# Performance work log

Hardware: AMD Instinct MI355X
Metric: run time of the kernel (lower is better)

The kernel has to match this reference:

```python
import jax, jax.numpy as jnp
import numpy as np

L, C, CZ, H = 2048, 512, 16, 16
D = C // H
EPS = 1e-5


def _ln(x, g, b):
    mu = jnp.mean(x, axis=-1, keepdims=True)
    var = jnp.var(x, axis=-1, keepdims=True)
    return (x - mu) * jax.lax.rsqrt(var + EPS) * g + b


def _adaln(x, cond, ln_g, ln_b, w, b):
    # cond: [C] -> scale/shift broadcast over L
    ss = cond @ w + b                      # [2C]
    scale, shift = ss[:C], ss[C:]
    return _ln(x, ln_g, ln_b) * (1.0 + scale) + shift


def setup_inputs() -> dict:
    key = jax.random.key(0)
    ks = jax.random.split(key, 16)
    s = 0.02
    return {
        "x": jax.random.normal(ks[0], (L, C), jnp.float32),
        "pair": jax.random.normal(ks[1], (L, L, CZ), jnp.float32),
        "time_cond": jax.random.normal(ks[2], (C,), jnp.float32),
        "ln1_g": jnp.ones((C,), jnp.float32),
        "ln1_b": jnp.zeros((C,), jnp.float32),
        "ada1_w": jax.random.normal(ks[3], (C, 2 * C), jnp.float32) * s,
        "ada1_b": jnp.zeros((2 * C,), jnp.float32),
        "Wq": jax.random.normal(ks[4], (C, C), jnp.float32) * s,
        "Wk": jax.random.normal(ks[5], (C, C), jnp.float32) * s,
        "Wv": jax.random.normal(ks[6], (C, C), jnp.float32) * s,
        "Wpb": jax.random.normal(ks[7], (CZ, H), jnp.float32) * s,
        "Wo": jax.random.normal(ks[8], (C, C), jnp.float32) * s,
        "bo": jnp.zeros((C,), jnp.float32),
        "ln2_g": jnp.ones((C,), jnp.float32),
        "ln2_b": jnp.zeros((C,), jnp.float32),
        "ada2_w": jax.random.normal(ks[9], (C, 2 * C), jnp.float32) * s,
        "ada2_b": jnp.zeros((2 * C,), jnp.float32),
        "W1": jax.random.normal(ks[10], (C, 4 * C), jnp.float32) * s,
        "b1": jnp.zeros((4 * C,), jnp.float32),
        "W2": jax.random.normal(ks[11], (4 * C, C), jnp.float32) * s,
        "b2": jnp.zeros((C,), jnp.float32),
    }


def reference(x, pair, time_cond, ln1_g, ln1_b, ada1_w, ada1_b,
              Wq, Wk, Wv, Wpb, Wo, bo,
              ln2_g, ln2_b, ada2_w, ada2_b, W1, b1, W2, b2):
    h = _adaln(x, time_cond, ln1_g, ln1_b, ada1_w, ada1_b)        # [L, C]
    q = (h @ Wq).reshape(L, H, D)
    k = (h @ Wk).reshape(L, H, D)
    v = (h @ Wv).reshape(L, H, D)
    scores = jnp.einsum('ihd,jhd->hij', q, k) / jnp.sqrt(jnp.float32(D))
    scores = scores + jnp.einsum('ijz,zh->hij', pair, Wpb)         # pair bias
    attn = jax.nn.softmax(scores, axis=-1)                          # [H, L, L]
    out = jnp.einsum('hij,jhd->ihd', attn, v).reshape(L, C)
    x = x + out @ Wo + bo
    h2 = _adaln(x, time_cond, ln2_g, ln2_b, ada2_w, ada2_b)
    ff = jax.nn.gelu(h2 @ W1 + b1, approximate=False) @ W2 + b2
    return x + ff
```

## Files before the change

kernel.cpp:

```cpp
#include <hip/hip_runtime.h>
#include <cstdint>
#include <cstddef>

typedef short s16x8 __attribute__((ext_vector_type(8)));
typedef short s16x4 __attribute__((ext_vector_type(4)));
typedef float f32x4 __attribute__((ext_vector_type(4)));

union U8 { s16x8 v; s16x4 h[2]; unsigned short e[8]; };

__device__ __forceinline__ float bf2f(unsigned short u) {
  union { unsigned u; float f; } x; x.u = ((unsigned)u) << 16; return x.f;
}
__device__ __forceinline__ unsigned short f2bf(float f) {
  union { float f; unsigned u; } x; x.f = f;
  unsigned r = x.u + 0x7fffu + ((x.u >> 16) & 1u);
  return (unsigned short)(r >> 16);
}
__device__ __forceinline__ float gelu_exact(float x) {
  return 0.5f * x * (1.f + erff(x * 0.70710678118654752f));
}

__global__ __launch_bounds__(256) void k_transpose_bf16(
    const float* __restrict__ src, unsigned short* __restrict__ dst, int K, int N) {
  __shared__ float tile[32][33];
  int k0 = blockIdx.x * 32, n0 = blockIdx.y * 32;
  int t = threadIdx.x;
  int tr = t >> 5, tc = t & 31;
#pragma unroll
  for (int r = 0; r < 4; ++r) {
    int row = tr + r * 8;
    tile[row][tc] = src[(size_t)(k0 + row) * N + n0 + tc];
  }
  __syncthreads();
#pragma unroll
  for (int r = 0; r < 4; ++r) {
    int row = tr + r * 8;
    dst[(size_t)(n0 + row) * K + k0 + tc] = f2bf(tile[tc][row]);
  }
}

__global__ __launch_bounds__(256) void k_transpose4(
    const float* __restrict__ w0, const float* __restrict__ w1,
    const float* __restrict__ w2, const float* __restrict__ w3,
    unsigned short* __restrict__ o0, unsigned short* __restrict__ o1,
    unsigned short* __restrict__ o2, unsigned short* __restrict__ o3) {
  __shared__ float tile[32][33];
  int z = blockIdx.z;
  const float* src = (z == 0) ? w0 : (z == 1) ? w1 : (z == 2) ? w2 : w3;
  unsigned short* dst = (z == 0) ? o0 : (z == 1) ? o1 : (z == 2) ? o2 : o3;
  int k0 = blockIdx.x * 32, n0 = blockIdx.y * 32;
  int t = threadIdx.x;
  int tr = t >> 5, tc = t & 31;
#pragma unroll
  for (int r = 0; r < 4; ++r) {
    int row = tr + r * 8;
    tile[row][tc] = src[(size_t)(k0 + row) * 512 + n0 + tc];
  }
  __syncthreads();
#pragma unroll
  for (int r = 0; r < 4; ++r) {
    int row = tr + r * 8;
    dst[(size_t)(n0 + row) * 512 + k0 + tc] = f2bf(tile[tc][row]);
  }
}

__global__ __launch_bounds__(256) void k_transpose_v(
    const unsigned short* __restrict__ qkv, unsigned short* __restrict__ vT) {
  __shared__ unsigned short tile[32][33];
  int j0 = blockIdx.x * 32, d0 = blockIdx.y * 32;
  int t = threadIdx.x;
  int tr = t >> 5, tc = t & 31;
#pragma unroll
  for (int r = 0; r < 4; ++r) {
    int row = tr + r * 8;
    tile[row][tc] = qkv[(size_t)(j0 + row) * 1536 + 1024 + d0 + tc];
  }
  __syncthreads();
#pragma unroll
  for (int r = 0; r < 4; ++r) {
    int row = tr + r * 8;
    vT[(size_t)(d0 + row) * 2048 + j0 + tc] = tile[tc][row];
  }
}

__global__ __launch_bounds__(256) void k_ada_ss(
    const float* __restrict__ tcv,
    const float* __restrict__ w1, const float* __restrict__ b1,
    const float* __restrict__ w2, const float* __restrict__ b2,
    float* __restrict__ ss) {
  int lane = threadIdx.x & 63;
  int kp = threadIdx.x >> 6;
  int jg = blockIdx.x * 64 + lane;
  int which = jg >> 10; int j = jg & 1023;
  const float* W = which ? w2 : w1;
  float acc = 0.f;
#pragma unroll 8
  for (int k = kp * 128; k < kp * 128 + 128; ++k)
    acc += tcv[k] * W[(size_t)k * 1024 + j];
  __shared__ float red[256];
  red[threadIdx.x] = acc;
  __syncthreads();
  if (kp == 0) {
    float v = red[lane] + red[64 + lane] + red[128 + lane] + red[192 + lane];
    v += (which ? b2 : b1)[j];
    ss[jg] = v;
  }
}

__global__ __launch_bounds__(256) void k_adaln(
    const float* __restrict__ x, const float* __restrict__ g,
    const float* __restrict__ b, const float* __restrict__ ss,
    unsigned short* __restrict__ out) {
  int row = blockIdx.x; int t = threadIdx.x;
  float2 v = ((const float2*)(x + (size_t)row * 512))[t];
  float s = v.x + v.y;
  float s2 = v.x * v.x + v.y * v.y;
#pragma unroll
  for (int off = 32; off >= 1; off >>= 1) {
    s += __shfl_xor(s, off);
    s2 += __shfl_xor(s2, off);
  }
  __shared__ float red[8];
  int wave = t >> 6, lane = t & 63;
  if (lane == 0) { red[wave] = s; red[4 + wave] = s2; }
  __syncthreads();
  float S = red[0] + red[1] + red[2] + red[3];
  float S2 = red[4] + red[5] + red[6] + red[7];
  float mu = S * (1.f / 512.f);
  float var = S2 * (1.f / 512.f) - mu * mu;
  float rs = rsqrtf(var + 1e-5f);
  int c0 = t * 2, c1 = t * 2 + 1;
  float h0 = ((v.x - mu) * rs * g[c0] + b[c0]) * (1.f + ss[c0]) + ss[512 + c0];
  float h1 = ((v.y - mu) * rs * g[c1] + b[c1]) * (1.f + ss[c1]) + ss[512 + c1];
  ushort2 o2; o2.x = f2bf(h0); o2.y = f2bf(h1);
  ((ushort2*)(out + (size_t)row * 512))[t] = o2;
}

template <int EPI>
__global__ __launch_bounds__(256) void k_gemm(
    const unsigned short* __restrict__ A, const unsigned short* __restrict__ Bt,
    const float* __restrict__ bias, const float* __restrict__ resid,
    void* __restrict__ out, int M, int N, int K) {
  __shared__ __align__(16) unsigned short As[64 * 68];
  __shared__ __align__(16) unsigned short Bs[64 * 68];
  int m0 = blockIdx.x * 64, n0 = blockIdx.y * 64;
  int t = threadIdx.x;
  int wave = t >> 6, lane = t & 63, q = lane >> 4, lid = lane & 15;
  f32x4 acc[4];
#pragma unroll
  for (int i = 0; i < 4; ++i) acc[i] = (f32x4){0.f, 0.f, 0.f, 0.f};
  int srow = t >> 2, scol = (t & 3) * 16;
  const unsigned short* ag = A + (size_t)(m0 + srow) * K + scol;
  const unsigned short* bg = Bt + (size_t)(n0 + srow) * K + scol;
  for (int k0 = 0; k0 < K; k0 += 64) {
    s16x8 av0 = *(const s16x8*)(ag + k0);
    s16x8 av1 = *(const s16x8*)(ag + k0 + 8);
    s16x8 bv0 = *(const s16x8*)(bg + k0);
    s16x8 bv1 = *(const s16x8*)(bg + k0 + 8);
    __syncthreads();
    *(s16x8*)&As[srow * 68 + scol] = av0;
    *(s16x8*)&As[srow * 68 + scol + 8] = av1;
    *(s16x8*)&Bs[srow * 68 + scol] = bv0;
    *(s16x8*)&Bs[srow * 68 + scol + 8] = bv1;
    __syncthreads();
#pragma unroll
    for (int ks = 0; ks < 64; ks += 32) {
      U8 bfr;
      bfr.h[0] = *(const s16x4*)&Bs[(wave * 16 + lid) * 68 + ks + q * 8];
      bfr.h[1] = *(const s16x4*)&Bs[(wave * 16 + lid) * 68 + ks + q * 8 + 4];
#pragma unroll
      for (int mf = 0; mf < 4; ++mf) {
        U8 afr;
        afr.h[0] = *(const s16x4*)&As[(mf * 16 + lid) * 68 + ks + q * 8];
        afr.h[1] = *(const s16x4*)&As[(mf * 16 + lid) * 68 + ks + q * 8 + 4];
        acc[mf] = __builtin_amdgcn_mfma_f32_16x16x32_bf16(afr.v, bfr.v, acc[mf], 0, 0, 0);
      }
    }
  }
  int col = n0 + wave * 16 + lid;
#pragma unroll
  for (int mf = 0; mf < 4; ++mf) {
#pragma unroll
    for (int r = 0; r < 4; ++r) {
      int row = m0 + mf * 16 + q * 4 + r;
      float v = acc[mf][r];
      if (EPI == 0) {
        ((unsigned short*)out)[(size_t)row * N + col] = f2bf(v);
      } else if (EPI == 1) {
        ((float*)out)[(size_t)row * N + col] = v + bias[col] + resid[(size_t)row * N + col];
      } else {
        ((unsigned short*)out)[(size_t)row * N + col] = f2bf(gelu_exact(v + bias[col]));
      }
    }
  }
}

#define BIAS_HS 1156
__global__ __launch_bounds__(512, 4) void k_attn(
    const unsigned short* __restrict__ qkv,
    const unsigned short* __restrict__ vT,
    const float* __restrict__ pair, const float* __restrict__ wpb,
    unsigned short* __restrict__ opart, float* __restrict__ lpart) {
  __shared__ __align__(16) unsigned short bias_lds[16 * BIAS_HS];
  __shared__ __align__(16) unsigned short p_lds[8 * 1152];

  const int jseg = blockIdx.x;
  const int iseg = blockIdx.y;
  const int ibase = iseg * 32;
  const int t = threadIdx.x;
  const int w = t >> 6, lane = t & 63, q = lane >> 4, lid = lane & 15;

  U8 wf;
#pragma unroll
  for (int e = 0; e < 8; ++e) {
    int k = q * 8 + e;
    wf.e[e] = (k < 16) ? (short)f2bf(wpb[k * 16 + lid]) : (short)0;
  }

  U8 aq[2][2];
#pragma unroll
  for (int hh = 0; hh < 2; ++hh) {
    int h = w * 2 + hh;
#pragma unroll
    for (int mf = 0; mf < 2; ++mf)
      aq[hh][mf].v = *(const s16x8*)(qkv + (size_t)(ibase + mf * 16 + lid) * 1536 + h * 32 + q * 8);
  }

  f32x4 o[2][2][2];
  float lsum[2][2][4];
#pragma unroll
  for (int a = 0; a < 2; ++a)
#pragma unroll
    for (int b = 0; b < 2; ++b) {
#pragma unroll
      for (int c = 0; c < 2; ++c) o[a][b][c] = (f32x4){0.f, 0.f, 0.f, 0.f};
#pragma unroll
      for (int r = 0; r < 4; ++r) lsum[a][b][r] = 0.f;
    }

  unsigned short* pP = p_lds + w * 1152;
  const float scale = 0.17677669529663687f;

#pragma unroll 1
  for (int jt = 0; jt < 8; ++jt) {
    const int jb = jseg * 256 + jt * 32;

    __syncthreads();

#pragma unroll
    for (int gc = 0; gc < 4; ++gc) {
      float4 pl[2][2];
#pragma unroll
      for (int gi = 0; gi < 2; ++gi) {
        int g = gc * 2 + gi;
        int ijrow = w * 128 + g * 16 + lid;
        int ii = ijrow >> 5, jj = ijrow & 31;
        const float* src = pair + ((size_t)(ibase + ii) * 2048 + (jb + jj)) * 16 + (q & 1) * 8;
        if (q < 2) { pl[gi][0] = *(const float4*)src; pl[gi][1] = *(const float4*)(src + 4); }
      }
#pragma unroll
      for (int gi = 0; gi < 2; ++gi) {
        int g = gc * 2 + gi;
        U8 af; af.v = (s16x8){0, 0, 0, 0, 0, 0, 0, 0};
        if (q < 2) {
          af.e[0] = f2bf(pl[gi][0].x); af.e[1] = f2bf(pl[gi][0].y);
          af.e[2] = f2bf(pl[gi][0].z); af.e[3] = f2bf(pl[gi][0].w);
          af.e[4] = f2bf(pl[gi][1].x); af.e[5] = f2bf(pl[gi][1].y);
          af.e[6] = f2bf(pl[gi][1].z); af.e[7] = f2bf(pl[gi][1].w);
        }
        f32x4 z = (f32x4){0.f, 0.f, 0.f, 0.f};
        f32x4 bacc = __builtin_amdgcn_mfma_f32_16x16x32_bf16(af.v, wf.v, z, 0, 0, 0);
        int il = (w << 2) + (g >> 1);
        int jlb = ((g & 1) << 4) + (q << 2);
        s16x4 bs;
        bs[0] = f2bf(bacc[0]); bs[1] = f2bf(bacc[1]);
        bs[2] = f2bf(bacc[2]); bs[3] = f2bf(bacc[3]);
        *(s16x4*)&bias_lds[lid * BIAS_HS + il * 36 + jlb] = bs;
      }
    }
    __syncthreads();

#pragma unroll
    for (int hh = 0; hh < 2; ++hh) {
      const int h = (w << 1) + hh;
      U8 bk[2], bv[2];
#pragma unroll
      for (int nf = 0; nf < 2; ++nf) {
        bk[nf].v = *(const s16x8*)(qkv + (size_t)(jb + nf * 16 + lid) * 1536 + 512 + h * 32 + q * 8);
        bv[nf].v = *(const s16x8*)(vT + (size_t)(h * 32 + nf * 16 + lid) * 2048 + jb + q * 8);
      }
      f32x4 z = (f32x4){0.f, 0.f, 0.f, 0.f};
      f32x4 s[2][2];
#pragma unroll
      for (int mf = 0; mf < 2; ++mf)
#pragma unroll
        for (int nf = 0; nf < 2; ++nf)
          s[mf][nf] = __builtin_amdgcn_mfma_f32_16x16x32_bf16(aq[hh][mf].v, bk[nf].v, z, 0, 0, 0);

      const unsigned short* brow = bias_lds + h * BIAS_HS;
#pragma unroll
      for (int mf = 0; mf < 2; ++mf) {
#pragma unroll
        for (int r = 0; r < 4; ++r) {
          int il = mf * 16 + (q << 2) + r;
          float b0 = bf2f(brow[il * 36 + lid]);
          float b1 = bf2f(brow[il * 36 + 16 + lid]);
          float p0 = __expf(fmaf(s[mf][0][r], scale, b0));
          float p1 = __expf(fmaf(s[mf][1][r], scale, b1));
          lsum[hh][mf][r] += p0 + p1;
          pP[il * 36 + lid] = f2bf(p0);
          pP[il * 36 + 16 + lid] = f2bf(p1);
        }
      }
      U8 aP[2];
#pragma unroll
      for (int mf = 0; mf < 2; ++mf) {
        aP[mf].h[0] = *(const s16x4*)&pP[(mf * 16 + lid) * 36 + q * 8];
        aP[mf].h[1] = *(const s16x4*)&pP[(mf * 16 + lid) * 36 + q * 8 + 4];
      }
#pragma unroll
      for (int nfd = 0; nfd < 2; ++nfd)
#pragma unroll
        for (int mf = 0; mf < 2; ++mf)
          o[hh][mf][nfd] = __builtin_amdgcn_mfma_f32_16x16x32_bf16(aP[mf].v, bv[nfd].v, o[hh][mf][nfd], 0, 0, 0);
    }
  }

#pragma unroll
  for (int hh = 0; hh < 2; ++hh) {
    int h = (w << 1) + hh;
#pragma unroll
    for (int mf = 0; mf < 2; ++mf) {
#pragma unroll
      for (int r = 0; r < 4; ++r) {
        float v = lsum[hh][mf][r];
        v += __shfl_xor(v, 1); v += __shfl_xor(v, 2);
        v += __shfl_xor(v, 4); v += __shfl_xor(v, 8);
        int i = ibase + mf * 16 + (q << 2) + r;
        if (lid == 0) lpart[((size_t)jseg * 2048 + i) * 16 + h] = v;
#pragma unroll
        for (int nfd = 0; nfd < 2; ++nfd)
          opart[((size_t)jseg * 2048 + i) * 512 + h * 32 + nfd * 16 + lid] = f2bf(o[hh][mf][nfd][r]);
      }
    }
  }
}

__global__ __launch_bounds__(512) void k_combine(
    const unsigned short* __restrict__ opart, const float* __restrict__ lpart,
    unsigned short* __restrict__ attn) {
  int i = blockIdx.x, t = threadIdx.x;
  int h = t >> 5;
  float den = 0.f, acc = 0.f;
#pragma unroll
  for (int s = 0; s < 8; ++s) {
    den += lpart[((size_t)s * 2048 + i) * 16 + h];
    acc += bf2f(opart[((size_t)s * 2048 + i) * 512 + t]);
  }
  attn[(size_t)i * 512 + t] = f2bf(acc / den);
}

extern "C" void kernel_launch(void* const* d_in, const int* in_sizes, int n_in,
                              void* d_out, int out_size, void* d_ws, size_t ws_size,
                              hipStream_t stream) {
  (void)in_sizes; (void)n_in; (void)out_size; (void)ws_size;
  const float* x      = (const float*)d_in[0];
  const float* pair   = (const float*)d_in[1];
  const float* tc     = (const float*)d_in[2];
  const float* ln1_g  = (const float*)d_in[3];
  const float* ln1_b  = (const float*)d_in[4];
  const float* ada1_w = (const float*)d_in[5];
  const float* ada1_b = (const float*)d_in[6];
  const float* Wq     = (const float*)d_in[7];
  const float* Wk     = (const float*)d_in[8];
  const float* Wv     = (const float*)d_in[9];
  const float* Wpb    = (const float*)d_in[10];
  const float* Wo     = (const float*)d_in[11];
  const float* bo     = (const float*)d_in[12];
  const float* ln2_g  = (const float*)d_in[13];
  const float* ln2_b  = (const float*)d_in[14];
  const float* ada2_w = (const float*)d_in[15];
  const float* ada2_b = (const float*)d_in[16];
  const float* W1     = (const float*)d_in[17];
  const float* b1     = (const float*)d_in[18];
  const float* W2     = (const float*)d_in[19];
  const float* b2     = (const float*)d_in[20];

  char* p = (char*)d_ws;
  auto alloc = [&](size_t bytes) {
    char* r = p;
    p += (bytes + 255) & ~(size_t)255;
    return r;
  };
  unsigned short* wqkv_t = (unsigned short*)alloc((size_t)1536 * 512 * 2);
  unsigned short* wo_t   = (unsigned short*)alloc((size_t)512 * 512 * 2);
  unsigned short* w1_t   = (unsigned short*)alloc((size_t)2048 * 512 * 2);
  unsigned short* w2_t   = (unsigned short*)alloc((size_t)512 * 2048 * 2);
  float*          ssb    = (float*)alloc((size_t)2048 * 4);
  unsigned short* h1     = (unsigned short*)alloc((size_t)2048 * 512 * 2);
  unsigned short* qkv    = (unsigned short*)alloc((size_t)2048 * 1536 * 2);
  unsigned short* vTb    = (unsigned short*)alloc((size_t)512 * 2048 * 2);
  unsigned short* opart  = (unsigned short*)alloc((size_t)8 * 2048 * 512 * 2);
  float*          lpb    = (float*)alloc((size_t)8 * 2048 * 16 * 4);
  unsigned short* attnb  = (unsigned short*)alloc((size_t)2048 * 512 * 2);
  float*          x2     = (float*)alloc((size_t)2048 * 512 * 4);
  unsigned short* h2     = (unsigned short*)alloc((size_t)2048 * 512 * 2);
  unsigned short* ffm    = (unsigned short*)alloc((size_t)2048 * 2048 * 2);

  k_transpose4<<<dim3(16, 16, 4), 256, 0, stream>>>(
      Wq, Wk, Wv, Wo, wqkv_t, wqkv_t + (size_t)512 * 512, wqkv_t + (size_t)1024 * 512, wo_t);
  k_transpose_bf16<<<dim3(16, 64), 256, 0, stream>>>(W1, w1_t, 512, 2048);
  k_transpose_bf16<<<dim3(64, 16), 256, 0, stream>>>(W2, w2_t, 2048, 512);

  k_ada_ss<<<32, 256, 0, stream>>>(tc, ada1_w, ada1_b, ada2_w, ada2_b, ssb);
  k_adaln<<<2048, 256, 0, stream>>>(x, ln1_g, ln1_b, ssb, h1);
  k_gemm<0><<<dim3(32, 24), 256, 0, stream>>>(h1, wqkv_t, nullptr, nullptr, qkv, 2048, 1536, 512);
  k_transpose_v<<<dim3(64, 16), 256, 0, stream>>>(qkv, vTb);
  k_attn<<<dim3(8, 64), 512, 0, stream>>>(qkv, vTb, pair, Wpb, opart, lpb);
  k_combine<<<2048, 512, 0, stream>>>(opart, lpb, attnb);
  k_gemm<1><<<dim3(32, 8), 256, 0, stream>>>(attnb, wo_t, bo, x, x2, 2048, 512, 512);
  k_adaln<<<2048, 256, 0, stream>>>(x2, ln2_g, ln2_b, ssb + 1024, h2);
  k_gemm<2><<<dim3(32, 32), 256, 0, stream>>>(h2, w1_t, b1, nullptr, ffm, 2048, 2048, 512);
  k_gemm<1><<<dim3(32, 8), 256, 0, stream>>>(ffm, w2_t, b2, x2, (float*)d_out, 2048, 512, 2048);
}
```

Measured before the change: 609.1 us.

## Prefetch pair bias, use 32x32 MFMA for bias, fuse V transpose into QKV GEMM

The GEMM kernel now runs 512 threads with a 128-wide K tile and register prefetch of the next K slice, overlapping global loads with MFMA work. The QKV GEMM epilogue writes the transposed V directly, which removes the separate transpose kernel launch. In attention, the pair-bias projection uses a 32x32x16 MFMA so no lanes are zeroed out, and the next tile's pair data is prefetched into registers during compute. The GEMM epilogue trades this for strided uncoalesced V-transpose stores, higher register pressure, and more LDS per block.

```diff
diff --git a/kernel.cpp b/kernel.cpp
--- a/kernel.cpp
+++ b/kernel.cpp
@@ -5,6 +5,7 @@
 typedef short s16x8 __attribute__((ext_vector_type(8)));
 typedef short s16x4 __attribute__((ext_vector_type(4)));
 typedef float f32x4 __attribute__((ext_vector_type(4)));
+typedef float f32x16 __attribute__((ext_vector_type(16)));
 
 union U8 { s16x8 v; s16x4 h[2]; unsigned short e[8]; };
 
@@ -61,25 +62,6 @@
   for (int r = 0; r < 4; ++r) {
     int row = tr + r * 8;
     dst[(size_t)(n0 + row) * 512 + k0 + tc] = f2bf(tile[tc][row]);
-  }
-}
-
-__global__ __launch_bounds__(256) void k_transpose_v(
-    const unsigned short* __restrict__ qkv, unsigned short* __restrict__ vT) {
-  __shared__ unsigned short tile[32][33];
-  int j0 = blockIdx.x * 32, d0 = blockIdx.y * 32;
-  int t = threadIdx.x;
-  int tr = t >> 5, tc = t & 31;
-#pragma unroll
-  for (int r = 0; r < 4; ++r) {
-    int row = tr + r * 8;
-    tile[row][tc] = qkv[(size_t)(j0 + row) * 1536 + 1024 + d0 + tc];
-  }
-  __syncthreads();
-#pragma unroll
-  for (int r = 0; r < 4; ++r) {
-    int row = tr + r * 8;
-    vT[(size_t)(d0 + row) * 2048 + j0 + tc] = tile[tc][row];
   }
 }
 
@@ -137,55 +119,66 @@
 }
 
 template <int EPI>
-__global__ __launch_bounds__(256) void k_gemm(
+__global__ __launch_bounds__(512, 4) void k_gemm(
     const unsigned short* __restrict__ A, const unsigned short* __restrict__ Bt,
     const float* __restrict__ bias, const float* __restrict__ resid,
-    void* __restrict__ out, int M, int N, int K) {
-  __shared__ __align__(16) unsigned short As[64 * 68];
-  __shared__ __align__(16) unsigned short Bs[64 * 68];
+    void* __restrict__ out, unsigned short* __restrict__ vt,
+    int M, int N, int K) {
+  __shared__ __align__(16) unsigned short As[64 * 132];
+  __shared__ __align__(16) unsigned short Bs[64 * 132];
   int m0 = blockIdx.x * 64, n0 = blockIdx.y * 64;
   int t = threadIdx.x;
-  int wave = t >> 6, lane = t & 63, q = lane >> 4, lid = lane & 15;
-  f32x4 acc[4];
-#pragma unroll
-  for (int i = 0; i < 4; ++i) acc[i] = (f32x4){0.f, 0.f, 0.f, 0.f};
-  int srow = t >> 2, scol = (t & 3) * 16;
+  int w = t >> 6, lane = t & 63, q = lane >> 4, lid = lane & 15;
+  int mhalf = w >> 2, nstrip = w & 3;
+  f32x4 acc[2];
+  acc[0] = (f32x4){0.f, 0.f, 0.f, 0.f};
+  acc[1] = (f32x4){0.f, 0.f, 0.f, 0.f};
+  int srow = t >> 3, scol = (t & 7) * 16;
   const unsigned short* ag = A + (size_t)(m0 + srow) * K + scol;
   const unsigned short* bg = Bt + (size_t)(n0 + srow) * K + scol;
-  for (int k0 = 0; k0 < K; k0 += 64) {
-    s16x8 av0 = *(const s16x8*)(ag + k0);
-    s16x8 av1 = *(const s16x8*)(ag + k0 + 8);
-    s16x8 bv0 = *(const s16x8*)(bg + k0);
-    s16x8 bv1 = *(const s16x8*)(bg + k0 + 8);
+  s16x8 av0 = *(const s16x8*)(ag);
+  s16x8 av1 = *(const s16x8*)(ag + 8);
+  s16x8 bv0 = *(const s16x8*)(bg);
+  s16x8 bv1 = *(const s16x8*)(bg + 8);
+  for (int k0 = 0; k0 < K; k0 += 128) {
     __syncthreads();
-    *(s16x8*)&As[srow * 68 + scol] = av0;
-    *(s16x8*)&As[srow * 68 + scol + 8] = av1;
-    *(s16x8*)&Bs[srow * 68 + scol] = bv0;
-    *(s16x8*)&Bs[srow * 68 + scol + 8] = bv1;
+    *(s16x8*)&As[srow * 132 + scol] = av0;
+    *(s16x8*)&As[srow * 132 + scol + 8] = av1;
+    *(s16x8*)&Bs[srow * 132 + scol] = bv0;
+    *(s16x8*)&Bs[srow * 132 + scol + 8] = bv1;
     __syncthreads();
-#pragma unroll
-    for (int ks = 0; ks < 64; ks += 32) {
+    if (k0 + 128 < K) {
+      av0 = *(const s16x8*)(ag + k0 + 128);
+      av1 = *(const s16x8*)(ag + k0 + 136);
+      bv0 = *(const s16x8*)(bg + k0 + 128);
+      bv1 = *(const s16x8*)(bg + k0 + 136);
+    }
+#pragma unroll
+    for (int ks = 0; ks < 128; ks += 32) {
       U8 bfr;
-      bfr.h[0] = *(const s16x4*)&Bs[(wave * 16 + lid) * 68 + ks + q * 8];
-      bfr.h[1] = *(const s16x4*)&Bs[(wave * 16 + lid) * 68 + ks + q * 8 + 4];
-#pragma unroll
-      for (int mf = 0; mf < 4; ++mf) {
+      bfr.h[0] = *(const s16x4*)&Bs[(nstrip * 16 + lid) * 132 + ks + q * 8];
+      bfr.h[1] = *(const s16x4*)&Bs[(nstrip * 16 + lid) * 132 + ks + q * 8 + 4];
+#pragma unroll
+      for (int mf = 0; mf < 2; ++mf) {
         U8 afr;
-        afr.h[0] = *(const s16x4*)&As[(mf * 16 + lid) * 68 + ks + q * 8];
-        afr.h[1] = *(const s16x4*)&As[(mf * 16 + lid) * 68 + ks + q * 8 + 4];
+        afr.h[0] = *(const s16x4*)&As[(mhalf * 32 + mf * 16 + lid) * 132 + ks + q * 8];
+        afr.h[1] = *(const s16x4*)&As[(mhalf * 32 + mf * 16 + lid) * 132 + ks + q * 8 + 4];
         acc[mf] = __builtin_amdgcn_mfma_f32_16x16x32_bf16(afr.v, bfr.v, acc[mf], 0, 0, 0);
       }
     }
   }
-  int col = n0 + wave * 16 + lid;
-#pragma unroll
-  for (int mf = 0; mf < 4; ++mf) {
+  int col = n0 + nstrip * 16 + lid;
+#pragma unroll
+  for (int mf = 0; mf < 2; ++mf) {
 #pragma unroll
     for (int r = 0; r < 4; ++r) {
-      int row = m0 + mf * 16 + q * 4 + r;
+      int row = m0 + mhalf * 32 + mf * 16 + q * 4 + r;
       float v = acc[mf][r];
       if (EPI == 0) {
-        ((unsigned short*)out)[(size_t)row * N + col] = f2bf(v);
+        unsigned short bv = f2bf(v);
+        ((unsigned short*)out)[(size_t)row * N + col] = bv;
+        if (vt != nullptr && col >= 1024)
+          vt[(size_t)(col - 1024) * 2048 + row] = bv;
       } else if (EPI == 1) {
         ((float*)out)[(size_t)row * N + col] = v + bias[col] + resid[(size_t)row * N + col];
       } else {
@@ -209,12 +202,13 @@
   const int ibase = iseg * 32;
   const int t = threadIdx.x;
   const int w = t >> 6, lane = t & 63, q = lane >> 4, lid = lane & 15;
+  const int hcol = lane & 31, khalf = lane >> 5;
 
   U8 wf;
 #pragma unroll
   for (int e = 0; e < 8; ++e) {
-    int k = q * 8 + e;
-    wf.e[e] = (k < 16) ? (short)f2bf(wpb[k * 16 + lid]) : (short)0;
+    int k = khalf * 8 + e;
+    wf.e[e] = (hcol < 16) ? (short)f2bf(wpb[k * 16 + hcol]) : (short)0;
   }
 
   U8 aq[2][2];
@@ -240,45 +234,61 @@
 
   unsigned short* pP = p_lds + w * 1152;
   const float scale = 0.17677669529663687f;
+
+  float4 pf[4][2];
+  {
+    const int jb0 = jseg * 256;
+#pragma unroll
+    for (int g = 0; g < 4; ++g) {
+      const float* src = pair + ((size_t)(ibase + w * 4 + g) * 2048 + (jb0 + hcol)) * 16 + khalf * 8;
+      pf[g][0] = *(const float4*)src;
+      pf[g][1] = *(const float4*)(src + 4);
+    }
+  }
 
 #pragma unroll 1
   for (int jt = 0; jt < 8; ++jt) {
     const int jb = jseg * 256 + jt * 32;
 
+    U8 af[4];
+#pragma unroll
+    for (int g = 0; g < 4; ++g) {
+      af[g].e[0] = f2bf(pf[g][0].x); af[g].e[1] = f2bf(pf[g][0].y);
+      af[g].e[2] = f2bf(pf[g][0].z); af[g].e[3] = f2bf(pf[g][0].w);
+      af[g].e[4] = f2bf(pf[g][1].x); af[g].e[5] = f2bf(pf[g][1].y);
+      af[g].e[6] = f2bf(pf[g][1].z); af[g].e[7] = f2bf(pf[g][1].w);
+    }
+
     __syncthreads();
 
 #pragma unroll
-    for (int gc = 0; gc < 4; ++gc) {
-      float4 pl[2][2];
-#pragma unroll
-      for (int gi = 0; gi < 2; ++gi) {
-        int g = gc * 2 + gi;
-        int ijrow = w * 128 + g * 16 + lid;
-        int ii = ijrow >> 5, jj = ijrow & 31;
-        const float* src = pair + ((size_t)(ibase + ii) * 2048 + (jb + jj)) * 16 + (q & 1) * 8;
-        if (q < 2) { pl[gi][0] = *(const float4*)src; pl[gi][1] = *(const float4*)(src + 4); }
-      }
-#pragma unroll
-      for (int gi = 0; gi < 2; ++gi) {
-        int g = gc * 2 + gi;
-        U8 af; af.v = (s16x8){0, 0, 0, 0, 0, 0, 0, 0};
-        if (q < 2) {
-          af.e[0] = f2bf(pl[gi][0].x); af.e[1] = f2bf(pl[gi][0].y);
-          af.e[2] = f2bf(pl[gi][0].z); af.e[3] = f2bf(pl[gi][0].w);
-          af.e[4] = f2bf(pl[gi][1].x); af.e[5] = f2bf(pl[gi][1].y);
-          af.e[6] = f2bf(pl[gi][1].z); af.e[7] = f2bf(pl[gi][1].w);
+    for (int g = 0; g < 4; ++g) {
+      f32x16 z16 = (f32x16){0.f, 0.f, 0.f, 0.f, 0.f, 0.f, 0.f, 0.f,
+                            0.f, 0.f, 0.f, 0.f, 0.f, 0.f, 0.f, 0.f};
+      f32x16 bacc = __builtin_amdgcn_mfma_f32_32x32x16_bf16(af[g].v, wf.v, bacc, 0, 0, 0);
+      bacc = __builtin_amdgcn_mfma_f32_32x32x16_bf16(af[g].v, wf.v, z16, 0, 0, 0);
+      if (hcol < 16) {
+        int base = hcol * BIAS_HS + (w * 4 + g) * 36;
+#pragma unroll
+        for (int rq = 0; rq < 4; ++rq) {
+          s16x4 bs;
+          bs[0] = f2bf(bacc[rq * 4 + 0]); bs[1] = f2bf(bacc[rq * 4 + 1]);
+          bs[2] = f2bf(bacc[rq * 4 + 2]); bs[3] = f2bf(bacc[rq * 4 + 3]);
+          *(s16x4*)&bias_lds[base + rq * 8 + khalf * 4] = bs;
         }
-        f32x4 z = (f32x4){0.f, 0.f, 0.f, 0.f};
-        f32x4 bacc = __builtin_amdgcn_mfma_f32_16x16x32_bf16(af.v, wf.v, z, 0, 0, 0);
-        int il = (w << 2) + (g >> 1);
-        int jlb = ((g & 1) << 4) + (q << 2);
-        s16x4 bs;
-        bs[0] = f2bf(bacc[0]); bs[1] = f2bf(bacc[1]);
-        bs[2] = f2bf(bacc[2]); bs[3] = f2bf(bacc[3]);
-        *(s16x4*)&bias_lds[lid * BIAS_HS + il * 36 + jlb] = bs;
       }
     }
     __syncthreads();
+
+    if (jt < 7) {
+      const int jbn = jb + 32;
+#pragma unroll
+      for (int g = 0; g < 4; ++g) {
+        const float* src = pair + ((size_t)(ibase + w * 4 + g) * 2048 + (jbn + hcol)) * 16 + khalf * 8;
+        pf[g][0] = *(const float4*)src;
+        pf[g][1] = *(const float4*)(src + 4);
+      }
+    }
 
 #pragma unroll
     for (int hh = 0; hh < 2; ++hh) {
@@ -414,12 +424,11 @@
 
   k_ada_ss<<<32, 256, 0, stream>>>(tc, ada1_w, ada1_b, ada2_w, ada2_b, ssb);
   k_adaln<<<2048, 256, 0, stream>>>(x, ln1_g, ln1_b, ssb, h1);
-  k_gemm<0><<<dim3(32, 24), 256, 0, stream>>>(h1, wqkv_t, nullptr, nullptr, qkv, 2048, 1536, 512);
-  k_transpose_v<<<dim3(64, 16), 256, 0, stream>>>(qkv, vTb);
+  k_gemm<0><<<dim3(32, 24), 512, 0, stream>>>(h1, wqkv_t, nullptr, nullptr, qkv, vTb, 2048, 1536, 512);
   k_attn<<<dim3(8, 64), 512, 0, stream>>>(qkv, vTb, pair, Wpb, opart, lpb);
   k_combine<<<2048, 512, 0, stream>>>(opart, lpb, attnb);
-  k_gemm<1><<<dim3(32, 8), 256, 0, stream>>>(attnb, wo_t, bo, x, x2, 2048, 512, 512);
+  k_gemm<1><<<dim3(32, 8), 512, 0, stream>>>(attnb, wo_t, bo, x, x2, nullptr, 2048, 512, 512);
   k_adaln<<<2048, 256, 0, stream>>>(x2, ln2_g, ln2_b, ssb + 1024, h2);
-  k_gemm<2><<<dim3(32, 32), 256, 0, stream>>>(h2, w1_t, b1, nullptr, ffm, 2048, 2048, 512);
-  k_gemm<1><<<dim3(32, 8), 256, 0, stream>>>(ffm, w2_t, b2, x2, (float*)d_out, 2048, 512, 2048);
-}
+  k_gemm<2><<<dim3(32, 32), 512, 0, stream>>>(h2, w1_t, b1, nullptr, ffm, nullptr, 2048, 2048, 512);
+  k_gemm<1><<<dim3(32, 8), 512, 0, stream>>>(ffm, w2_t, b2, x2, (float*)d_out, nullptr, 2048, 512, 2048);
+}
```

New measurement: 598.7 us. About the same (-1.7%).
